# Performance work log

Measured on AMD Instinct MI355X. Metric: run time of the kernel, lower is better.

The kernel has to match this reference:

```python
import jax, jax.numpy as jnp
import numpy as np

N_NODES = 100000
NODES_PER_GRAPH = 200
N_GRAPHS = N_NODES // NODES_PER_GRAPH  # 500
N_EDGES = 3200000
NUM_FEATURES = 128
HIDDEN = 32
K_POOL = 50
NUM_CLASSES = 10
NUM_ITERATIONS = 3


def setup_inputs() -> dict:
    key = jax.random.key(0)
    ks = jax.random.split(key, 12)
    x = jax.random.normal(ks[0], (N_NODES, NUM_FEATURES), dtype=jnp.float32)
    edge_index = jax.random.randint(ks[1], (2, N_EDGES), 0, N_NODES, dtype=jnp.int64)
    batch = (jnp.arange(N_NODES, dtype=jnp.int64) // NODES_PER_GRAPH)
    # GCN weights (glorot-ish scale) + biases
    W1 = jax.random.normal(ks[2], (NUM_FEATURES, HIDDEN), dtype=jnp.float32) * (1.0 / np.sqrt(NUM_FEATURES))
    b1 = jnp.zeros((HIDDEN,), dtype=jnp.float32)
    W2 = jax.random.normal(ks[3], (HIDDEN, HIDDEN), dtype=jnp.float32) * (1.0 / np.sqrt(HIDDEN))
    b2 = jnp.zeros((HIDDEN,), dtype=jnp.float32)
    W3 = jax.random.normal(ks[4], (HIDDEN, HIDDEN), dtype=jnp.float32) * (1.0 / np.sqrt(HIDDEN))
    b3 = jnp.zeros((HIDDEN,), dtype=jnp.float32)
    # Capsule weights: [out_capsules, in_capsules, out_length, in_length]
    Wc1 = jax.random.normal(ks[5], (16, K_POOL, 32, 3 * HIDDEN), dtype=jnp.float32) * 0.05
    Wc2 = jax.random.normal(ks[6], (NUM_CLASSES, 16, 16, 32), dtype=jnp.float32) * 0.05
    return {"x": x, "edge_index": edge_index, "batch": batch,
            "W1": W1, "b1": b1, "W2": W2, "b2": b2, "W3": W3, "b3": b3,
            "Wc1": Wc1, "Wc2": Wc2}


def _gcn_conv(x, W, b, src, dst, mask):
    # PyG GCNConv: remove self-loops already done (mask), add self-loops, sym-normalize.
    h = x @ W  # [N, H]
    deg = jnp.zeros((x.shape[0],), dtype=h.dtype).at[dst].add(mask) + 1.0  # self-loop adds 1
    dinv = jax.lax.rsqrt(deg)
    norm = dinv[src] * dinv[dst] * mask  # [E]
    agg = jnp.zeros_like(h).at[dst].add(norm[:, None] * h[src])
    agg = agg + h * (dinv * dinv)[:, None]  # self-loop contribution h_i / deg_i
    return agg + b


def _squash(s, axis=-1):
    sq = jnp.sum(s * s, axis=axis, keepdims=True)
    return (sq / (1.0 + sq)) * s * jax.lax.rsqrt(sq + 1e-12)


def _capsule_linear(u, W, num_iterations):
    # u: [B, I, in_len]; W: [O, I, out_len, in_len]
    priors = jnp.einsum('oiLl,bil->boiL', W, u)  # [B, O, I, out_len]
    logits = jnp.zeros(priors.shape[:3] + (1,), dtype=priors.dtype)
    for it in range(num_iterations):
        c = jax.nn.softmax(logits, axis=1)             # over out capsules
        s = jnp.sum(c * priors, axis=2)                # [B, O, out_len]
        v = _squash(s)
        if it < num_iterations - 1:
            logits = logits + jnp.sum(priors * v[:, :, None, :], axis=-1, keepdims=True)
    return v


def _global_sort_pool(x, k):
    # x: [N, C], equal-size graphs -> [B, nper, C]; sort desc by last channel, take top-k
    xg = x.reshape(N_GRAPHS, NODES_PER_GRAPH, x.shape[-1])
    order = jnp.argsort(-xg[:, :, -1], axis=1)[:, :k]  # [B, k]
    return jnp.take_along_axis(xg, order[:, :, None], axis=1)  # [B, k, C]


def reference(x, edge_index, batch, W1, b1, W2, b2, W3, b3, Wc1, Wc2):
    src, dst = edge_index[0], edge_index[1]
    mask = (src != dst).astype(x.dtype)  # remove_self_loops
    x1 = jnp.tanh(_gcn_conv(x, W1, b1, src, dst, mask))
    x2 = jnp.tanh(_gcn_conv(x1, W2, b2, src, dst, mask))
    x3 = jnp.tanh(_gcn_conv(x2, W3, b3, src, dst, mask))
    xc = jnp.concatenate([x1, x2, x3], axis=-1)        # [N, 96]
    pooled = _global_sort_pool(xc, K_POOL)             # [B, 50, 96]
    out = _capsule_linear(pooled, Wc1, NUM_ITERATIONS)  # [B, 16, 32]
    out = _capsule_linear(out, Wc2, NUM_ITERATIONS)     # [B, 10, 16]
    return jnp.linalg.norm(out, axis=-1)                # [B, 10]
```

## Files before the change

kernel.cpp:

```cpp
#include <hip/hip_runtime.h>

#define NNODES 100000
#define NEDGES 3200000
#define NPG 200
#define NGRAPH 500
#define FIN 128
#define HID 32
#define KP 50
#define NCLS 10

#define NB1 196
#define BSH 9
#define CHUNK 8192
#define NBLK1 391
#define CAP 17408

__global__ __launch_bounds__(512) void k_place1(const int* __restrict__ src,
                                                const int* __restrict__ dst,
                                                int* __restrict__ cursor,
                                                unsigned* __restrict__ csorted) {
    __shared__ int hist[NB1];
    __shared__ int lstart[NB1];
    __shared__ int base[NB1];
    __shared__ int cnt2[NB1];
    __shared__ int sarr[256];
    __shared__ unsigned buf[CHUNK];
    __shared__ int dbuf[CHUNK];
    int t = threadIdx.x;
    for (int i = t; i < NB1; i += 512) { hist[i] = 0; cnt2[i] = 0; }
    __syncthreads();
    int eb = blockIdx.x * CHUNK;
    for (int i = 0; i < CHUNK / 512; ++i) {
        int e = eb + t + i * 512;
        if (e < NEDGES) {
            int s = src[e], d = dst[e];
            if (s != d) atomicAdd(&hist[d >> BSH], 1);
        }
    }
    __syncthreads();
    if (t < 256) sarr[t] = (t < NB1) ? hist[t] : 0;
    __syncthreads();
    for (int ofs = 1; ofs < 256; ofs <<= 1) {
        int add = (t < 256 && t >= ofs) ? sarr[t - ofs] : 0;
        __syncthreads();
        if (t < 256) sarr[t] += add;
        __syncthreads();
    }
    if (t < NB1) {
        lstart[t] = (t == 0) ? 0 : sarr[t - 1];
        base[t] = hist[t] ? (t * CAP + atomicAdd(&cursor[t], hist[t])) : 0;
    }
    __syncthreads();
    for (int i = 0; i < CHUNK / 512; ++i) {
        int e = eb + t + i * 512;
        if (e < NEDGES) {
            int s = src[e], d = dst[e];
            if (s != d) {
                int bk = d >> BSH;
                int pos = atomicAdd(&cnt2[bk], 1);
                int slot = lstart[bk] + pos;
                buf[slot] = ((unsigned)s << BSH) | (unsigned)(d & 511);
                dbuf[slot] = base[bk] + pos;
            }
        }
    }
    __syncthreads();
    int nval = sarr[NB1 - 1];
    for (int j = t; j < nval; j += 512) csorted[dbuf[j]] = buf[j];
}

__global__ __launch_bounds__(512) void k_fill2(const int* __restrict__ cursor,
                                               const unsigned* __restrict__ csorted,
                                               int* __restrict__ csrc,
                                               int2* __restrict__ begend,
                                               float* __restrict__ dinv) {
    __shared__ int cnt[512];
    __shared__ int loffs[512];
    __shared__ int cnt2[512];
    __shared__ int sarr[512];
    int b = blockIdx.x, t = threadIdx.x;
    cnt[t] = 0; cnt2[t] = 0;
    __syncthreads();
    int base = b * CAP;
    int m = cursor[b];
    for (int j = t; j < m; j += 512) atomicAdd(&cnt[csorted[base + j] & 511], 1);
    __syncthreads();
    sarr[t] = cnt[t];
    __syncthreads();
    for (int ofs = 1; ofs < 512; ofs <<= 1) {
        int add = (t >= ofs) ? sarr[t - ofs] : 0;
        __syncthreads();
        sarr[t] += add;
        __syncthreads();
    }
    loffs[t] = sarr[t] - cnt[t];
    __syncthreads();
    int n = b * 512 + t;
    if (n < NNODES) {
        int beg = base + loffs[t];
        begend[n] = make_int2(beg, beg + cnt[t]);
        dinv[n] = rsqrtf((float)cnt[t] + 1.0f);
    }
    for (int j = t; j < m; j += 512) {
        unsigned p = csorted[base + j];
        int d = p & 511;
        int pos = atomicAdd(&cnt2[d], 1);
        csrc[base + loffs[d] + pos] = (int)(p >> BSH);
    }
}

__global__ __launch_bounds__(256) void k_matmul(const float* __restrict__ X, int ldx, int K,
                                                const float* __restrict__ W,
                                                const float* __restrict__ dinv,
                                                float* __restrict__ h) {
    __shared__ float Xk[32 * 256];
    __shared__ float Wl[32 * 36];
    int t = threadIdx.x;
    int tx = t & 7;
    int ty = t >> 3;
    int n0 = blockIdx.x * 256;
    float acc[8][4];
#pragma unroll
    for (int r = 0; r < 8; ++r)
#pragma unroll
        for (int c = 0; c < 4; ++c) acc[r][c] = 0.f;

    int ksteps = K >> 5;
    for (int ks = 0; ks < ksteps; ++ks) {
        int kbase = ks << 5;
        __syncthreads();
        for (int idx = t; idx < 256 * 8; idx += 256) {
            int row = idx >> 3, c4 = (idx & 7) * 4;
            float4 v = make_float4(0.f, 0.f, 0.f, 0.f);
            if (n0 + row < NNODES)
                v = *reinterpret_cast<const float4*>(X + (size_t)(n0 + row) * ldx + kbase + c4);
            float vv[4] = {v.x, v.y, v.z, v.w};
#pragma unroll
            for (int j = 0; j < 4; ++j) {
                int k = c4 + j;
                int gp = (row >> 2) ^ ((k >> 2) & 31);
                Xk[k * 256 + gp * 4 + (row & 3)] = vv[j];
            }
        }
        for (int idx = t; idx < 32 * 32; idx += 256) {
            int k = idx >> 5, j = idx & 31;
            Wl[k * 36 + j] = W[(size_t)(kbase + k) * HID + j];
        }
        __syncthreads();
        const float4* Xq = reinterpret_cast<const float4*>(Xk);
        const float4* Wq = reinterpret_cast<const float4*>(Wl);
        for (int k = 0; k < 32; ++k) {
            int key = (k >> 2) & 31;
            float4 a0 = Xq[k * 64 + (ty ^ key)];
            float4 a1 = Xq[k * 64 + 32 + (ty ^ key)];
            float4 wv = Wq[k * 9 + tx];
            float a[8] = {a0.x, a0.y, a0.z, a0.w, a1.x, a1.y, a1.z, a1.w};
#pragma unroll
            for (int r = 0; r < 8; ++r) {
                acc[r][0] += a[r] * wv.x;
                acc[r][1] += a[r] * wv.y;
                acc[r][2] += a[r] * wv.z;
                acc[r][3] += a[r] * wv.w;
            }
        }
    }
#pragma unroll
    for (int r = 0; r < 8; ++r) {
        int row = (r < 4) ? (4 * ty + r) : (128 + 4 * ty + (r - 4));
        int gr = n0 + row;
        if (gr < NNODES) {
            float di = dinv[gr];
            float4 v = make_float4(acc[r][0] * di, acc[r][1] * di, acc[r][2] * di, acc[r][3] * di);
            *reinterpret_cast<float4*>(h + (size_t)gr * HID + 4 * tx) = v;
        }
    }
}

__global__ __launch_bounds__(256) void k_gather(const int2* __restrict__ begend,
                                                const int* __restrict__ csrc,
                                                const float* __restrict__ dinv,
                                                const float* __restrict__ hw,
                                                const float* __restrict__ bias,
                                                float* __restrict__ xc, int coloff) {
    int t = threadIdx.x;
    int wv = t >> 6;
    int lane = t & 63;
    int nh = lane >> 5;
    int sub = lane & 31;
    int g = sub >> 3;
    int q = sub & 7;
    int n = blockIdx.x * 8 + wv * 2 + nh;
    int2 be = begend[n];
    int beg = be.x, end = be.y, last = end - 1;
    float4 acc = make_float4(0.f, 0.f, 0.f, 0.f);
    int e0 = beg + g;
    for (; e0 + 28 < end; e0 += 32) {
#pragma unroll
        for (int j = 0; j < 8; ++j) {
            int s = csrc[e0 + 4 * j];
            float4 hv = *reinterpret_cast<const float4*>(hw + (size_t)s * HID + q * 4);
            acc.x += hv.x; acc.y += hv.y; acc.z += hv.z; acc.w += hv.w;
        }
    }
    if (e0 < end) {
#pragma unroll
        for (int j = 0; j < 8; ++j) {
            int e = e0 + 4 * j;
            float mk = (e <= last) ? 1.f : 0.f;
            int s = csrc[min(e, last)];
            float4 hv = *reinterpret_cast<const float4*>(hw + (size_t)s * HID + q * 4);
            acc.x += mk * hv.x; acc.y += mk * hv.y; acc.z += mk * hv.z; acc.w += mk * hv.w;
        }
    }
    for (int m = 8; m <= 16; m <<= 1) {
        acc.x += __shfl_xor(acc.x, m, 64);
        acc.y += __shfl_xor(acc.y, m, 64);
        acc.z += __shfl_xor(acc.z, m, 64);
        acc.w += __shfl_xor(acc.w, m, 64);
    }
    if (g == 0) {
        float di = dinv[n];
        float4 hv = *reinterpret_cast<const float4*>(hw + (size_t)n * HID + q * 4);
        float4 bv = *reinterpret_cast<const float4*>(bias + q * 4);
        float4 v;
        v.x = tanhf(di * (acc.x + hv.x) + bv.x);
        v.y = tanhf(di * (acc.y + hv.y) + bv.y);
        v.z = tanhf(di * (acc.z + hv.z) + bv.z);
        v.w = tanhf(di * (acc.w + hv.w) + bv.w);
        *reinterpret_cast<float4*>(xc + (size_t)n * 96 + coloff + q * 4) = v;
    }
}

__global__ __launch_bounds__(256) void k_sortpool(const float* __restrict__ xc,
                                                  float* __restrict__ pooled) {
    int g = blockIdx.x;
    __shared__ float vals[NPG];
    __shared__ int sel[KP];
    int t = threadIdx.x;
    if (t < NPG) vals[t] = xc[((size_t)g * NPG + t) * 96 + 95];
    __syncthreads();
    if (t < NPG) {
        float v = vals[t];
        int r = 0;
        for (int k = 0; k < NPG; ++k) {
            float vk = vals[k];
            r += (vk > v) || (vk == v && k < t);
        }
        if (r < KP) sel[r] = t;
    }
    __syncthreads();
    for (int idx = t; idx < KP * 24; idx += 256) {
        int r = idx / 24, c4 = (idx % 24) * 4;
        *reinterpret_cast<float4*>(pooled + (size_t)g * KP * 96 + r * 96 + c4) =
            *reinterpret_cast<const float4*>(xc + ((size_t)g * NPG + sel[r]) * 96 + c4);
    }
}

__global__ __launch_bounds__(512, 2) void k_priors1(const float* __restrict__ pooled,
                                                    const float* __restrict__ Wc1,
                                                    float* __restrict__ priors) {
    int bid = blockIdx.x;
    int ct = bid & 3;
    int bt = (bid >> 2) & 1;
    int i = bid >> 3;
    __shared__ float As[48 * 256];
    __shared__ float Bs[48 * 128];
    int t = threadIdx.x;
    int tx = t & 15, ty = t >> 4;
    float acc[8][8];
#pragma unroll
    for (int r = 0; r < 8; ++r)
#pragma unroll
        for (int c = 0; c < 8; ++c) acc[r][c] = 0.f;

    for (int kh = 0; kh < 2; ++kh) {
        int kbase = kh * 48;
        __syncthreads();
        for (int idx = t; idx < 256 * 12; idx += 512) {
            int r = idx / 12, c4 = (idx % 12) * 4;
            int b = bt * 256 + r;
            float4 v = make_float4(0.f, 0.f, 0.f, 0.f);
            if (b < NGRAPH)
                v = *reinterpret_cast<const float4*>(pooled + ((size_t)b * KP + i) * 96 + kbase + c4);
            float vv[4] = {v.x, v.y, v.z, v.w};
#pragma unroll
            for (int j = 0; j < 4; ++j) {
                int k = c4 + j;
                int gp = (r >> 2) ^ ((k >> 2) & 31);
                As[k * 256 + gp * 4 + (r & 3)] = vv[j];
            }
        }
        for (int idx = t; idx < 128 * 12; idx += 512) {
            int c = idx / 12, c4 = (idx % 12) * 4;
            int col = ct * 128 + c;
            const float* wr = Wc1 + (((size_t)(col >> 5) * KP + i) * 32 + (col & 31)) * 96;
            float4 v = *reinterpret_cast<const float4*>(wr + kbase + c4);
            float vv[4] = {v.x, v.y, v.z, v.w};
#pragma unroll
            for (int j = 0; j < 4; ++j) {
                int k = c4 + j;
                int gp = (c >> 2) ^ ((k >> 2) & 31);
                Bs[k * 128 + gp * 4 + (c & 3)] = vv[j];
            }
        }
        __syncthreads();
        for (int k = 0; k < 48; ++k) {
            int key = (k >> 2) & 31;
            float4 a0 = *reinterpret_cast<const float4*>(&As[k * 256 + 4 * (ty ^ key)]);
            float4 a1 = *reinterpret_cast<const float4*>(&As[k * 256 + 4 * ((32 + ty) ^ key)]);
            float4 b0 = *reinterpret_cast<const float4*>(&Bs[k * 128 + 4 * (tx ^ key)]);
            float4 b1 = *reinterpret_cast<const float4*>(&Bs[k * 128 + 4 * ((16 + tx) ^ key)]);
            float a[8] = {a0.x, a0.y, a0.z, a0.w, a1.x, a1.y, a1.z, a1.w};
            float bb[8] = {b0.x, b0.y, b0.z, b0.w, b1.x, b1.y, b1.z, b1.w};
#pragma unroll
            for (int r = 0; r < 8; ++r)
#pragma unroll
                for (int c = 0; c < 8; ++c) acc[r][c] += a[r] * bb[c];
        }
    }
#pragma unroll
    for (int rh = 0; rh < 2; ++rh)
#pragma unroll
        for (int rr = 0; rr < 4; ++rr) {
            int b = bt * 256 + rh * 128 + ty * 4 + rr;
            if (b >= NGRAPH) continue;
#pragma unroll
            for (int ch = 0; ch < 2; ++ch) {
                int col = ct * 128 + ch * 64 + tx * 4;
                int o = col >> 5, L = col & 31;
                float4 v = make_float4(acc[rh * 4 + rr][ch * 4 + 0],
                                       acc[rh * 4 + rr][ch * 4 + 1],
                                       acc[rh * 4 + rr][ch * 4 + 2],
                                       acc[rh * 4 + rr][ch * 4 + 3]);
                *reinterpret_cast<float4*>(priors + (((size_t)b * 16 + o) * KP + i) * 32 + L) = v;
            }
        }
}

__global__ __launch_bounds__(256) void k_routing1(const float* __restrict__ priors_g,
                                                  float* __restrict__ v_out) {
    int b = blockIdx.x;
    __shared__ float P[16 * KP * 33];
    __shared__ float logits[16 * KP];
    __shared__ float c[16 * KP];
    __shared__ float s[16 * 32];
    __shared__ float v[16 * 32];
    __shared__ float scale[16];
    int t = threadIdx.x;
    const float* pg = priors_g + (size_t)b * (16 * KP * 32);
    for (int idx = t; idx < 16 * KP * 32; idx += 256)
        P[(idx >> 5) * 33 + (idx & 31)] = pg[idx];
    for (int idx = t; idx < 16 * KP; idx += 256) logits[idx] = 0.f;
    __syncthreads();
    for (int it = 0; it < 3; ++it) {
        if (t < KP) {
            float m = -1e30f;
            for (int o = 0; o < 16; ++o) m = fmaxf(m, logits[o * KP + t]);
            float sum = 0.f;
            for (int o = 0; o < 16; ++o) {
                float e = expf(logits[o * KP + t] - m);
                c[o * KP + t] = e;
                sum += e;
            }
            for (int o = 0; o < 16; ++o) c[o * KP + t] /= sum;
        }
        __syncthreads();
        for (int idx = t; idx < 16 * 32; idx += 256) {
            int o = idx >> 5, L = idx & 31;
            float acc = 0.f;
            for (int i = 0; i < KP; ++i) acc += c[o * KP + i] * P[(o * KP + i) * 33 + L];
            s[idx] = acc;
        }
        __syncthreads();
        if (t < 16) {
            float sq = 0.f;
            for (int L = 0; L < 32; ++L) sq += s[t * 32 + L] * s[t * 32 + L];
            scale[t] = (sq / (1.f + sq)) * (1.0f / sqrtf(sq + 1e-12f));
        }
        __syncthreads();
        for (int idx = t; idx < 16 * 32; idx += 256) v[idx] = s[idx] * scale[idx >> 5];
        __syncthreads();
        if (it < 2) {
            for (int idx = t; idx < 16 * KP; idx += 256) {
                int o = idx / KP, i = idx % KP;
                float acc = 0.f;
                for (int L = 0; L < 32; ++L) acc += P[(o * KP + i) * 33 + L] * v[o * 32 + L];
                logits[idx] += acc;
            }
            __syncthreads();
        }
    }
    for (int idx = t; idx < 16 * 32; idx += 256) v_out[(size_t)b * 512 + idx] = v[idx];
}

__global__ __launch_bounds__(256) void k_caps2(const float* __restrict__ v1,
                                               const float* __restrict__ Wc2,
                                               float* __restrict__ out) {
    int b = blockIdx.x;
    __shared__ float ul[16 * 32];
    __shared__ float P[NCLS * 16 * 17];
    __shared__ float logits[NCLS * 16];
    __shared__ float c[NCLS * 16];
    __shared__ float s[NCLS * 16];
    __shared__ float v[NCLS * 16];
    __shared__ float scale[NCLS];
    int t = threadIdx.x;
    for (int idx = t; idx < 512; idx += 256) ul[idx] = v1[(size_t)b * 512 + idx];
    for (int idx = t; idx < NCLS * 16; idx += 256) logits[idx] = 0.f;
    __syncthreads();
    for (int idx = t; idx < NCLS * 16 * 16; idx += 256) {
        int L = idx & 15, i = (idx >> 4) & 15, o = idx >> 8;
        const float4* wr = reinterpret_cast<const float4*>(Wc2 + ((size_t)((o * 16 + i) * 16 + L)) * 32);
        const float4* ur = reinterpret_cast<const float4*>(&ul[i * 32]);
        float acc = 0.f;
#pragma unroll
        for (int l = 0; l < 8; ++l) {
            float4 w4 = wr[l], u4 = ur[l];
            acc += w4.x * u4.x + w4.y * u4.y + w4.z * u4.z + w4.w * u4.w;
        }
        P[(idx >> 4) * 17 + L] = acc;
    }
    __syncthreads();
    for (int it = 0; it < 3; ++it) {
        if (t < 16) {
            float m = -1e30f;
            for (int o = 0; o < NCLS; ++o) m = fmaxf(m, logits[o * 16 + t]);
            float sum = 0.f;
            for (int o = 0; o < NCLS; ++o) {
                float e = expf(logits[o * 16 + t] - m);
                c[o * 16 + t] = e;
                sum += e;
            }
            for (int o = 0; o < NCLS; ++o) c[o * 16 + t] /= sum;
        }
        __syncthreads();
        if (t < NCLS * 16) {
            int o = t >> 4, L = t & 15;
            float acc = 0.f;
            for (int i = 0; i < 16; ++i) acc += c[o * 16 + i] * P[(o * 16 + i) * 17 + L];
            s[t] = acc;
        }
        __syncthreads();
        if (t < NCLS) {
            float sq = 0.f;
            for (int L = 0; L < 16; ++L) sq += s[t * 16 + L] * s[t * 16 + L];
            scale[t] = (sq / (1.f + sq)) * (1.0f / sqrtf(sq + 1e-12f));
        }
        __syncthreads();
        if (t < NCLS * 16) v[t] = s[t] * scale[t >> 4];
        __syncthreads();
        if (it < 2) {
            if (t < NCLS * 16) {
                int o = t >> 4, i = t & 15;
                float acc = 0.f;
                for (int L = 0; L < 16; ++L) acc += P[(o * 16 + i) * 17 + L] * v[o * 16 + L];
                logits[t] += acc;
            }
            __syncthreads();
        }
    }
    if (t < NCLS) {
        float sq = 0.f;
        for (int L = 0; L < 16; ++L) sq += v[t * 16 + L] * v[t * 16 + L];
        out[(size_t)b * NCLS + t] = sqrtf(sq);
    }
}

extern "C" void kernel_launch(void* const* d_in, const int* in_sizes, int n_in,
                              void* d_out, int out_size, void* d_ws, size_t ws_size,
                              hipStream_t stream) {
    const float* x   = (const float*)d_in[0];
    const int*   ei  = (const int*)d_in[1];
    const float* W1  = (const float*)d_in[3];
    const float* b1  = (const float*)d_in[4];
    const float* W2  = (const float*)d_in[5];
    const float* b2  = (const float*)d_in[6];
    const float* W3  = (const float*)d_in[7];
    const float* b3  = (const float*)d_in[8];
    const float* Wc1 = (const float*)d_in[9];
    const float* Wc2 = (const float*)d_in[10];
    float* out = (float*)d_out;
    float* wsf = (float*)d_ws;

    const int* src = ei;
    const int* dst = ei + NEDGES;

    float* xc = wsf;
    float* R  = wsf + 9600000;
    int*   cursor  = (int*)R;
    float* dinv    = R + 256;
    int2*  begend  = (int2*)(R + 100256);
    float* A       = R + 300256;
    unsigned* csorted = (unsigned*)A;
    float* h       = A;
    float* pooled  = A;
    int*   csrc    = (int*)(R + 3712224);
    float* pr1     = R + 7124192;
    float* v1      = R + 19924192;

    hipMemsetAsync(cursor, 0, 256 * sizeof(int), stream);
    k_place1<<<NBLK1, 512, 0, stream>>>(src, dst, cursor, csorted);
    k_fill2<<<NB1, 512, 0, stream>>>(cursor, csorted, csrc, begend, dinv);

    k_matmul<<<(NNODES + 255) / 256, 256, 0, stream>>>(x, FIN, FIN, W1, dinv, h);
    k_gather<<<NNODES / 8, 256, 0, stream>>>(begend, csrc, dinv, h, b1, xc, 0);
    k_matmul<<<(NNODES + 255) / 256, 256, 0, stream>>>(xc, 96, HID, W2, dinv, h);
    k_gather<<<NNODES / 8, 256, 0, stream>>>(begend, csrc, dinv, h, b2, xc, 32);
    k_matmul<<<(NNODES + 255) / 256, 256, 0, stream>>>(xc + 32, 96, HID, W3, dinv, h);
    k_gather<<<NNODES / 8, 256, 0, stream>>>(begend, csrc, dinv, h, b3, xc, 64);

    k_sortpool<<<NGRAPH, 256, 0, stream>>>(xc, pooled);
    k_priors1<<<KP * 8, 512, 0, stream>>>(pooled, Wc1, pr1);
    k_routing1<<<NGRAPH, 256, 0, stream>>>(pr1, v1);
    k_caps2<<<NGRAPH, 256, 0, stream>>>(v1, Wc2, out);
}
```

Measured before the change: 371.7 us.

## Prefetch second K-half into registers in priors GEMM and fuse capsule kernels

In the capsule priors GEMM, the global loads for the second K half now go into registers before the first half's FMA loop runs, so memory latency overlaps with compute (register-staged double buffering). Separately, the first routing kernel and the second capsule layer are merged into one kernel, removing a launch and the round trip of v1 through global memory. The cost is higher register pressure in the GEMM and more shared memory in the fused kernel, which may lower occupancy.

Result: no change. 376.1 us (+1.2%).

```diff
diff --git a/kernel.cpp b/kernel.cpp
--- a/kernel.cpp
+++ b/kernel.cpp
@@ -273,50 +273,118 @@
 #pragma unroll
         for (int c = 0; c < 8; ++c) acc[r][c] = 0.f;
 
-    for (int kh = 0; kh < 2; ++kh) {
-        int kbase = kh * 48;
-        __syncthreads();
-        for (int idx = t; idx < 256 * 12; idx += 512) {
-            int r = idx / 12, c4 = (idx % 12) * 4;
-            int b = bt * 256 + r;
-            float4 v = make_float4(0.f, 0.f, 0.f, 0.f);
-            if (b < NGRAPH)
-                v = *reinterpret_cast<const float4*>(pooled + ((size_t)b * KP + i) * 96 + kbase + c4);
-            float vv[4] = {v.x, v.y, v.z, v.w};
-#pragma unroll
-            for (int j = 0; j < 4; ++j) {
-                int k = c4 + j;
-                int gp = (r >> 2) ^ ((k >> 2) & 31);
-                As[k * 256 + gp * 4 + (r & 3)] = vv[j];
-            }
-        }
-        for (int idx = t; idx < 128 * 12; idx += 512) {
-            int c = idx / 12, c4 = (idx % 12) * 4;
-            int col = ct * 128 + c;
-            const float* wr = Wc1 + (((size_t)(col >> 5) * KP + i) * 32 + (col & 31)) * 96;
-            float4 v = *reinterpret_cast<const float4*>(wr + kbase + c4);
-            float vv[4] = {v.x, v.y, v.z, v.w};
-#pragma unroll
-            for (int j = 0; j < 4; ++j) {
-                int k = c4 + j;
-                int gp = (c >> 2) ^ ((k >> 2) & 31);
-                Bs[k * 128 + gp * 4 + (c & 3)] = vv[j];
-            }
-        }
-        __syncthreads();
-        for (int k = 0; k < 48; ++k) {
-            int key = (k >> 2) & 31;
-            float4 a0 = *reinterpret_cast<const float4*>(&As[k * 256 + 4 * (ty ^ key)]);
-            float4 a1 = *reinterpret_cast<const float4*>(&As[k * 256 + 4 * ((32 + ty) ^ key)]);
-            float4 b0 = *reinterpret_cast<const float4*>(&Bs[k * 128 + 4 * (tx ^ key)]);
-            float4 b1 = *reinterpret_cast<const float4*>(&Bs[k * 128 + 4 * ((16 + tx) ^ key)]);
-            float a[8] = {a0.x, a0.y, a0.z, a0.w, a1.x, a1.y, a1.z, a1.w};
-            float bb[8] = {b0.x, b0.y, b0.z, b0.w, b1.x, b1.y, b1.z, b1.w};
-#pragma unroll
-            for (int r = 0; r < 8; ++r)
-#pragma unroll
-                for (int c = 0; c < 8; ++c) acc[r][c] += a[r] * bb[c];
-        }
+    float4 ra[6], rb[3];
+#pragma unroll
+    for (int u = 0; u < 6; ++u) {
+        int idx = t + 512 * u;
+        int r = idx / 12, c4 = (idx % 12) * 4;
+        int b = bt * 256 + r;
+        ra[u] = make_float4(0.f, 0.f, 0.f, 0.f);
+        if (b < NGRAPH)
+            ra[u] = *reinterpret_cast<const float4*>(pooled + ((size_t)b * KP + i) * 96 + c4);
+    }
+#pragma unroll
+    for (int u = 0; u < 3; ++u) {
+        int idx = t + 512 * u;
+        int c = idx / 12, c4 = (idx % 12) * 4;
+        int col = ct * 128 + c;
+        rb[u] = *reinterpret_cast<const float4*>(
+            Wc1 + (((size_t)(col >> 5) * KP + i) * 32 + (col & 31)) * 96 + c4);
+    }
+#pragma unroll
+    for (int u = 0; u < 6; ++u) {
+        int idx = t + 512 * u;
+        int r = idx / 12, c4 = (idx % 12) * 4;
+        float vv[4] = {ra[u].x, ra[u].y, ra[u].z, ra[u].w};
+#pragma unroll
+        for (int j = 0; j < 4; ++j) {
+            int k = c4 + j;
+            int gp = (r >> 2) ^ ((k >> 2) & 31);
+            As[k * 256 + gp * 4 + (r & 3)] = vv[j];
+        }
+    }
+#pragma unroll
+    for (int u = 0; u < 3; ++u) {
+        int idx = t + 512 * u;
+        int c = idx / 12, c4 = (idx % 12) * 4;
+        float vv[4] = {rb[u].x, rb[u].y, rb[u].z, rb[u].w};
+#pragma unroll
+        for (int j = 0; j < 4; ++j) {
+            int k = c4 + j;
+            int gp = (c >> 2) ^ ((k >> 2) & 31);
+            Bs[k * 128 + gp * 4 + (c & 3)] = vv[j];
+        }
+    }
+    __syncthreads();
+    float4 ra2[6], rb2[3];
+#pragma unroll
+    for (int u = 0; u < 6; ++u) {
+        int idx = t + 512 * u;
+        int r = idx / 12, c4 = (idx % 12) * 4;
+        int b = bt * 256 + r;
+        ra2[u] = make_float4(0.f, 0.f, 0.f, 0.f);
+        if (b < NGRAPH)
+            ra2[u] = *reinterpret_cast<const float4*>(pooled + ((size_t)b * KP + i) * 96 + 48 + c4);
+    }
+#pragma unroll
+    for (int u = 0; u < 3; ++u) {
+        int idx = t + 512 * u;
+        int c = idx / 12, c4 = (idx % 12) * 4;
+        int col = ct * 128 + c;
+        rb2[u] = *reinterpret_cast<const float4*>(
+            Wc1 + (((size_t)(col >> 5) * KP + i) * 32 + (col & 31)) * 96 + 48 + c4);
+    }
+    for (int k = 0; k < 48; ++k) {
+        int key = (k >> 2) & 31;
+        float4 a0 = *reinterpret_cast<const float4*>(&As[k * 256 + 4 * (ty ^ key)]);
+        float4 a1 = *reinterpret_cast<const float4*>(&As[k * 256 + 4 * ((32 + ty) ^ key)]);
+        float4 b0 = *reinterpret_cast<const float4*>(&Bs[k * 128 + 4 * (tx ^ key)]);
+        float4 b1 = *reinterpret_cast<const float4*>(&Bs[k * 128 + 4 * ((16 + tx) ^ key)]);
+        float a[8] = {a0.x, a0.y, a0.z, a0.w, a1.x, a1.y, a1.z, a1.w};
+        float bb[8] = {b0.x, b0.y, b0.z, b0.w, b1.x, b1.y, b1.z, b1.w};
+#pragma unroll
+        for (int r = 0; r < 8; ++r)
+#pragma unroll
+            for (int c = 0; c < 8; ++c) acc[r][c] += a[r] * bb[c];
+    }
+    __syncthreads();
+#pragma unroll
+    for (int u = 0; u < 6; ++u) {
+        int idx = t + 512 * u;
+        int r = idx / 12, c4 = (idx % 12) * 4;
+        float vv[4] = {ra2[u].x, ra2[u].y, ra2[u].z, ra2[u].w};
+#pragma unroll
+        for (int j = 0; j < 4; ++j) {
+            int k = c4 + j;
+            int gp = (r >> 2) ^ ((k >> 2) & 31);
+            As[k * 256 + gp * 4 + (r & 3)] = vv[j];
+        }
+    }
+#pragma unroll
+    for (int u = 0; u < 3; ++u) {
+        int idx = t + 512 * u;
+        int c = idx / 12, c4 = (idx % 12) * 4;
+        float vv[4] = {rb2[u].x, rb2[u].y, rb2[u].z, rb2[u].w};
+#pragma unroll
+        for (int j = 0; j < 4; ++j) {
+            int k = c4 + j;
+            int gp = (c >> 2) ^ ((k >> 2) & 31);
+            Bs[k * 128 + gp * 4 + (c & 3)] = vv[j];
+        }
+    }
+    __syncthreads();
+    for (int k = 0; k < 48; ++k) {
+        int key = (k >> 2) & 31;
+        float4 a0 = *reinterpret_cast<const float4*>(&As[k * 256 + 4 * (ty ^ key)]);
+        float4 a1 = *reinterpret_cast<const float4*>(&As[k * 256 + 4 * ((32 + ty) ^ key)]);
+        float4 b0 = *reinterpret_cast<const float4*>(&Bs[k * 128 + 4 * (tx ^ key)]);
+        float4 b1 = *reinterpret_cast<const float4*>(&Bs[k * 128 + 4 * ((16 + tx) ^ key)]);
+        float a[8] = {a0.x, a0.y, a0.z, a0.w, a1.x, a1.y, a1.z, a1.w};
+        float bb[8] = {b0.x, b0.y, b0.z, b0.w, b1.x, b1.y, b1.z, b1.w};
+#pragma unroll
+        for (int r = 0; r < 8; ++r)
+#pragma unroll
+            for (int c = 0; c < 8; ++c) acc[r][c] += a[r] * bb[c];
     }
 #pragma unroll
     for (int rh = 0; rh < 2; ++rh)
@@ -337,8 +405,9 @@
         }
 }
 
-__global__ __launch_bounds__(256) void k_routing1(const float* __restrict__ priors_g,
-                                                  float* __restrict__ v_out) {
+__global__ __launch_bounds__(256) void k_caps(const float* __restrict__ priors_g,
+                                              const float* __restrict__ Wc2,
+                                              float* __restrict__ out) {
     int b = blockIdx.x;
     __shared__ float P[16 * KP * 33];
     __shared__ float logits[16 * KP];
@@ -346,6 +415,12 @@
     __shared__ float s[16 * 32];
     __shared__ float v[16 * 32];
     __shared__ float scale[16];
+    __shared__ float P2[NCLS * 16 * 17];
+    __shared__ float logits2[NCLS * 16];
+    __shared__ float c2[NCLS * 16];
+    __shared__ float s2[NCLS * 16];
+    __shared__ float v2[NCLS * 16];
+    __shared__ float scale2[NCLS];
     int t = threadIdx.x;
     const float* pg = priors_g + (size_t)b * (16 * KP * 32);
     for (int idx = t; idx < 16 * KP * 32; idx += 256)
@@ -390,78 +465,61 @@
             __syncthreads();
         }
     }
-    for (int idx = t; idx < 16 * 32; idx += 256) v_out[(size_t)b * 512 + idx] = v[idx];
-}
-
-__global__ __launch_bounds__(256) void k_caps2(const float* __restrict__ v1,
-                                               const float* __restrict__ Wc2,
-                                               float* __restrict__ out) {
-    int b = blockIdx.x;
-    __shared__ float ul[16 * 32];
-    __shared__ float P[NCLS * 16 * 17];
-    __shared__ float logits[NCLS * 16];
-    __shared__ float c[NCLS * 16];
-    __shared__ float s[NCLS * 16];
-    __shared__ float v[NCLS * 16];
-    __shared__ float scale[NCLS];
-    int t = threadIdx.x;
-    for (int idx = t; idx < 512; idx += 256) ul[idx] = v1[(size_t)b * 512 + idx];
-    for (int idx = t; idx < NCLS * 16; idx += 256) logits[idx] = 0.f;
-    __syncthreads();
+    for (int idx = t; idx < NCLS * 16; idx += 256) logits2[idx] = 0.f;
     for (int idx = t; idx < NCLS * 16 * 16; idx += 256) {
         int L = idx & 15, i = (idx >> 4) & 15, o = idx >> 8;
         const float4* wr = reinterpret_cast<const float4*>(Wc2 + ((size_t)((o * 16 + i) * 16 + L)) * 32);
-        const float4* ur = reinterpret_cast<const float4*>(&ul[i * 32]);
+        const float4* ur = reinterpret_cast<const float4*>(&v[i * 32]);
         float acc = 0.f;
 #pragma unroll
         for (int l = 0; l < 8; ++l) {
             float4 w4 = wr[l], u4 = ur[l];
             acc += w4.x * u4.x + w4.y * u4.y + w4.z * u4.z + w4.w * u4.w;
         }
-        P[(idx >> 4) * 17 + L] = acc;
+        P2[(idx >> 4) * 17 + L] = acc;
     }
     __syncthreads();
     for (int it = 0; it < 3; ++it) {
         if (t < 16) {
             float m = -1e30f;
-            for (int o = 0; o < NCLS; ++o) m = fmaxf(m, logits[o * 16 + t]);
+            for (int o = 0; o < NCLS; ++o) m = fmaxf(m, logits2[o * 16 + t]);
             float sum = 0.f;
             for (int o = 0; o < NCLS; ++o) {
-                float e = expf(logits[o * 16 + t] - m);
-                c[o * 16 + t] = e;
+                float e = expf(logits2[o * 16 + t] - m);
+                c2[o * 16 + t] = e;
                 sum += e;
             }
-            for (int o = 0; o < NCLS; ++o) c[o * 16 + t] /= sum;
+            for (int o = 0; o < NCLS; ++o) c2[o * 16 + t] /= sum;
         }
         __syncthreads();
         if (t < NCLS * 16) {
             int o = t >> 4, L = t & 15;
             float acc = 0.f;
-            for (int i = 0; i < 16; ++i) acc += c[o * 16 + i] * P[(o * 16 + i) * 17 + L];
-            s[t] = acc;
+            for (int i = 0; i < 16; ++i) acc += c2[o * 16 + i] * P2[(o * 16 + i) * 17 + L];
+            s2[t] = acc;
         }
         __syncthreads();
         if (t < NCLS) {
             float sq = 0.f;
-            for (int L = 0; L < 16; ++L) sq += s[t * 16 + L] * s[t * 16 + L];
-            scale[t] = (sq / (1.f + sq)) * (1.0f / sqrtf(sq + 1e-12f));
-        }
-        __syncthreads();
-        if (t < NCLS * 16) v[t] = s[t] * scale[t >> 4];
+            for (int L = 0; L < 16; ++L) sq += s2[t * 16 + L] * s2[t * 16 + L];
+            scale2[t] = (sq / (1.f + sq)) * (1.0f / sqrtf(sq + 1e-12f));
+        }
+        __syncthreads();
+        if (t < NCLS * 16) v2[t] = s2[t] * scale2[t >> 4];
         __syncthreads();
         if (it < 2) {
             if (t < NCLS * 16) {
                 int o = t >> 4, i = t & 15;
                 float acc = 0.f;
-                for (int L = 0; L < 16; ++L) acc += P[(o * 16 + i) * 17 + L] * v[o * 16 + L];
-                logits[t] += acc;
+                for (int L = 0; L < 16; ++L) acc += P2[(o * 16 + i) * 17 + L] * v2[o * 16 + L];
+                logits2[t] += acc;
             }
             __syncthreads();
         }
     }
     if (t < NCLS) {
         float sq = 0.f;
-        for (int L = 0; L < 16; ++L) sq += v[t * 16 + L] * v[t * 16 + L];
+        for (int L = 0; L < 16; ++L) sq += v2[t * 16 + L] * v2[t * 16 + L];
         out[(size_t)b * NCLS + t] = sqrtf(sq);
     }
 }
@@ -496,7 +554,6 @@
     float* pooled  = A;
     int*   csrc    = (int*)(R + 3712224);
     float* pr1     = R + 7124192;
-    float* v1      = R + 19924192;
 
     hipMemsetAsync(cursor, 0, 256 * sizeof(int), stream);
     k_place1<<<NBLK1, 512, 0, stream>>>(src, dst, cursor, csorted);
@@ -511,6 +568,5 @@
 
     k_sortpool<<<NGRAPH, 256, 0, stream>>>(xc, pooled);
     k_priors1<<<KP * 8, 512, 0, stream>>>(pooled, Wc1, pr1);
-    k_routing1<<<NGRAPH, 256, 0, stream>>>(pr1, v1);
-    k_caps2<<<NGRAPH, 256, 0, stream>>>(v1, Wc2, out);
-}
+    k_caps<<<NGRAPH, 256, 0, stream>>>(pr1, Wc2, out);
+}
```
